# Performance work log

Hardware: AMD Instinct MI355X
Metric: run time of the kernel (lower is better)

Reference implementation:

```python
import jax, jax.numpy as jnp
import numpy as np

OUT_IMG = 256
OUT_MSK = 64


def _src_coords(n_out, size):
    # F.interpolate bilinear align_corners=False source coordinates, clamped to edge
    sizef = size.astype(jnp.float32)
    t = (jnp.arange(n_out, dtype=jnp.float32) + 0.5) * (sizef / n_out) - 0.5
    t = jnp.clip(t, 0.0, sizef - 1.0)
    t0 = jnp.floor(t).astype(jnp.int32)
    t1 = jnp.minimum(t0 + 1, size - 1)
    return t0, t1, t - t0.astype(jnp.float32)


def _per_sample(x_img, x_msk, x_bg, pad, sel, color):
    # x_img [3,H,W] float, x_msk [H,W] bool, x_bg [3,Hb,Wb], pad [4] int (l,r,t,b)
    H, W = x_msk.shape
    ys = jnp.any(x_msk, axis=1)
    xs = jnp.any(x_msk, axis=0)
    iy = jnp.arange(H)
    ix = jnp.arange(W)
    miny = jnp.min(jnp.where(ys, iy, H))
    maxy = jnp.max(jnp.where(ys, iy, -1))
    minx = jnp.min(jnp.where(xs, ix, W))
    maxx = jnp.max(jnp.where(xs, ix, -1))
    h = maxy - miny + 1
    w = maxx - minx + 1
    left, right, top, bot = pad[0], pad[1], pad[2], pad[3]
    Hp = h + top + bot   # padded crop height
    Wp = w + left + right  # padded crop width
    # background: real bg image or solid random color (c[ii][-1] > 2 branch)
    bg_sel = jnp.where(sel > 2, x_bg, jnp.broadcast_to(color[:, None, None], x_bg.shape))

    def mask_at(P, Q):
        # value of the padded-cropped mask at integer padded coords (P, Q)
        in_crop = (P >= top) & (P < top + h) & (Q >= left) & (Q < left + w)
        r = jnp.clip(miny + P - top, 0, H - 1)
        c = jnp.clip(minx + Q - left, 0, W - 1)
        return in_crop & x_msk[r, c], r, c

    def sample_img(py, px):
        # composited padded image at integer coords (py x px grid) -> [3,Ho,Wo]
        P = py[:, None]
        Q = px[None, :]
        m, r, c = mask_at(P, Q)
        iv = x_img[:, r, c]
        bv = bg_sel[:, P, Q]
        return jnp.where(m[None], iv, bv)

    def sample_msk(py, px):
        m, _, _ = mask_at(py[:, None], px[None, :])
        return m.astype(jnp.float32)

    def bilinear(sample_fn, n_out, ch_leading):
        y0, y1, wy = _src_coords(n_out, Hp)
        x0, x1, wx = _src_coords(n_out, Wp)
        s00 = sample_fn(y0, x0)
        s01 = sample_fn(y0, x1)
        s10 = sample_fn(y1, x0)
        s11 = sample_fn(y1, x1)
        wy_ = wy[:, None]
        wx_ = wx[None, :]
        if ch_leading:
            wy_ = wy_[None]
            wx_ = wx_[None]
        top_row = s00 * (1.0 - wx_) + s01 * wx_
        bot_row = s10 * (1.0 - wx_) + s11 * wx_
        return top_row * (1.0 - wy_) + bot_row * wy_

    img_out = bilinear(sample_img, OUT_IMG, True)        # [3,256,256]
    msk_out = bilinear(sample_msk, OUT_MSK, False)[None]  # [1,64,64]
    return img_out, msk_out


def _rgb_to_hsv(x):
    r, g, b = x[:, 0], x[:, 1], x[:, 2]
    mx = jnp.max(x, axis=1)
    mn = jnp.min(x, axis=1)
    d = mx - mn
    ds = jnp.where(d > 0, d, 1.0)
    hr = ((g - b) / ds) % 6.0
    hg = (b - r) / ds + 2.0
    hb = (r - g) / ds + 4.0
    hch = jnp.where(mx == r, hr, jnp.where(mx == g, hg, hb)) / 6.0
    hch = jnp.where(d > 0, hch, 0.0)
    s = jnp.where(mx > 0, d / jnp.where(mx > 0, mx, 1.0), 0.0)
    return hch, s, mx


def _hsv_to_rgb(hch, s, v):
    h6 = hch * 6.0
    i = jnp.floor(h6)
    f = h6 - i
    p = v * (1.0 - s)
    q = v * (1.0 - f * s)
    t = v * (1.0 - (1.0 - f) * s)
    im = i.astype(jnp.int32) % 6
    conds = [im == 0, im == 1, im == 2, im == 3, im == 4, im == 5]
    r = jnp.select(conds, [v, q, p, p, t, v])
    g = jnp.select(conds, [t, v, v, q, p, p])
    b = jnp.select(conds, [p, p, t, v, v, q])
    return jnp.stack([r, g, b], axis=1)


def _color_jitter(img, jit):
    # ColorJitter(0.1, 0.1, 0.1, 0.1) with explicit per-sample factors
    b = (0.9 + 0.2 * jit[:, 0])[:, None, None, None]
    c = (0.9 + 0.2 * jit[:, 1])[:, None, None, None]
    s = (0.9 + 0.2 * jit[:, 2])[:, None, None, None]
    hd = (-0.1 + 0.2 * jit[:, 3])[:, None, None]
    img = jnp.clip(img * b, 0.0, 1.0)
    gray = (0.299 * img[:, 0] + 0.587 * img[:, 1] + 0.114 * img[:, 2])[:, None]
    mean = jnp.mean(gray, axis=(2, 3), keepdims=True)
    img = jnp.clip(c * img + (1.0 - c) * mean, 0.0, 1.0)
    gray = (0.299 * img[:, 0] + 0.587 * img[:, 1] + 0.114 * img[:, 2])[:, None]
    img = jnp.clip(s * img + (1.0 - s) * gray, 0.0, 1.0)
    hch, sa, v = _rgb_to_hsv(img)
    hch = (hch + hd) % 1.0
    return jnp.clip(_hsv_to_rgb(hch, sa, v), 0.0, 1.0)


def setup_inputs() -> dict:
    key = jax.random.key(0)
    ks = jax.random.split(key, 7)
    B, H, W = 64, 448, 448
    return {
        "img": jax.random.uniform(ks[0], (B, 3, H, W), jnp.float32),
        "ms": jax.random.uniform(ks[1], (B, 1, H, W), jnp.float32),
        "bg": jax.random.uniform(ks[2], (B, 3, H + 40, W + 40), jnp.float32),
        "pads": jax.random.randint(ks[3], (B, 4), 0, 20, jnp.int32),
        "csel": jax.random.randint(ks[4], (B,), 0, 20, jnp.int32),
        "rand_color": jax.random.uniform(ks[5], (B, 3), jnp.float32),
        "jitter": jax.random.uniform(ks[6], (B, 4), jnp.float32),
    }


def reference(img, ms, bg, pads, csel, rand_color, jitter):
    mask = ms[:, 0] > 0.5
    img_out, msk_out = jax.vmap(_per_sample)(img, mask, bg, pads, csel, rand_color)
    img_out = _color_jitter(img_out, jitter)
    return img_out, msk_out
```

## Files before the change

kernel.cpp:

```cpp
#include <hip/hip_runtime.h>

#define H_IN 448
#define W_IN 448
#define HW_IN (H_IN * W_IN)
#define BGW 488
#define BGHW (BGW * BGW)
#define OUTI 256
#define OUTI_PIX (OUTI * OUTI)
#define OUTM 64
#define B_SAMPLES 64
#define BBOX_CHUNKS 16
#define BBOX_ROWS (H_IN / BBOX_CHUNKS)
#define BITS_STRIDE 8

typedef unsigned long long u64;

__device__ __forceinline__ float clamp01(float x) { return fminf(fmaxf(x, 0.f), 1.f); }
__device__ __forceinline__ int clampi(int x, int lo, int hi) { return min(max(x, lo), hi); }

__global__ void k_bbox(const float* __restrict__ ms, int* __restrict__ bbox,
                       u64* __restrict__ bits) {
    int b = blockIdx.y, chunk = blockIdx.x;
    int tid = threadIdx.x;
    int wave = tid >> 6, lane = tid & 63;
    const float* msB = ms + (size_t)b * HW_IN;
    u64* bitsB = bits + (size_t)b * H_IN * BITS_STRIDE;

    int miny = H_IN, maxy = -1, minx = W_IN, maxx = -1;
    for (int rr = wave; rr < BBOX_ROWS; rr += 4) {
        int row = chunk * BBOX_ROWS + rr;
        const float4* rowp = (const float4*)(msB + (size_t)row * W_IN);
#pragma unroll
        for (int sub = 0; sub < 2; ++sub) {
            int c4 = sub * 64 + lane;
            bool valid = c4 < (W_IN / 4);
            float4 v = rowp[min(c4, W_IN / 4 - 1)];
            bool a0 = valid && (v.x > 0.5f);
            bool a1 = valid && (v.y > 0.5f);
            bool a2 = valid && (v.z > 0.5f);
            bool a3 = valid && (v.w > 0.5f);
            u64 b0 = __ballot(a0), b1 = __ballot(a1), b2 = __ballot(a2), b3 = __ballot(a3);
            if (a0 | a1 | a2 | a3) {
                miny = min(miny, row); maxy = max(maxy, row);
                int xb = c4 * 4;
                if (a0) { minx = min(minx, xb);     maxx = max(maxx, xb); }
                if (a1) { minx = min(minx, xb + 1); maxx = max(maxx, xb + 1); }
                if (a2) { minx = min(minx, xb + 2); maxx = max(maxx, xb + 2); }
                if (a3) { minx = min(minx, xb + 3); maxx = max(maxx, xb + 3); }
            }
            if (lane < 4) {
                u64 w = (lane == 0) ? b0 : (lane == 1) ? b1 : (lane == 2) ? b2 : b3;
                bitsB[(size_t)row * BITS_STRIDE + sub * 4 + lane] = w;
            }
        }
    }
    __shared__ int s[4];
    if (tid == 0) { s[0] = H_IN; s[1] = -1; s[2] = W_IN; s[3] = -1; }
    __syncthreads();
    atomicMin(&s[0], miny); atomicMax(&s[1], maxy);
    atomicMin(&s[2], minx); atomicMax(&s[3], maxx);
    __syncthreads();
    if (tid == 0) {
        atomicMin(&bbox[b * 4 + 0], s[0]);
        atomicMin(&bbox[b * 4 + 1], -s[1]);
        atomicMin(&bbox[b * 4 + 2], s[2]);
        atomicMin(&bbox[b * 4 + 3], -s[3]);
    }
}

struct Geo {
    int miny, minx, h, w, top, left, Hp, Wp;
};
__device__ __forceinline__ Geo load_geo(const int* __restrict__ bbox,
                                        const int* __restrict__ pads, int b) {
    Geo g;
    g.miny = bbox[b * 4 + 0];
    int maxy = -bbox[b * 4 + 1];
    g.minx = bbox[b * 4 + 2];
    int maxx = -bbox[b * 4 + 3];
    int left = pads[b * 4 + 0], right = pads[b * 4 + 1];
    int top = pads[b * 4 + 2], bot = pads[b * 4 + 3];
    g.h = maxy - g.miny + 1;
    g.w = maxx - g.minx + 1;
    g.top = top; g.left = left;
    g.Hp = g.h + top + bot;
    g.Wp = g.w + left + right;
    return g;
}

__device__ __forceinline__ void src_coord(int i, int n_out, int size,
                                          int& t0, int& t1, float& frac) {
    float sizef = (float)size;
    float t = (i + 0.5f) * (sizef / (float)n_out) - 0.5f;
    t = fminf(fmaxf(t, 0.f), sizef - 1.f);
    t0 = (int)floorf(t);
    t1 = min(t0 + 1, size - 1);
    frac = t - (float)t0;
}

__device__ __forceinline__ bool mask_bit(const u64* rowbits, int c) {
    u64 w = rowbits[((c >> 8) << 2) | (c & 3)];
    return (w >> ((c >> 2) & 63)) & 1ULL;
}

__global__ void __launch_bounds__(256) k_resize_img(
        const float* __restrict__ img, const float* __restrict__ bg,
        const int* __restrict__ pads, const int* __restrict__ csel,
        const float* __restrict__ rcol, const float* __restrict__ jit,
        const int* __restrict__ bbox, const u64* __restrict__ bits,
        float* __restrict__ out, float* __restrict__ partials) {
    int oy = blockIdx.x;
    int ch = blockIdx.y;
    int b = blockIdx.z;
    int tid = threadIdx.x;

    Geo g = load_geo(bbox, pads, b);
    bool useBg = csel[b] > 2;
    float colv = rcol[b * 3 + ch];
    float bfac = 0.9f + 0.2f * jit[b * 4 + 0];

    int y0, y1; float wy;
    src_coord(oy, OUTI, g.Hp, y0, y1, wy);
    int r0 = clampi(g.miny + y0 - g.top, 0, H_IN - 1);
    int r1 = clampi(g.miny + y1 - g.top, 0, H_IN - 1);
    bool incy0 = (y0 >= g.top) && (y0 < g.top + g.h);
    bool incy1 = (y1 >= g.top) && (y1 < g.top + g.h);

    __shared__ float s_im[2][W_IN];
    __shared__ float s_bg[2][BGW];
    __shared__ u64 s_bits[2][BITS_STRIDE];

    const float* imC = img + ((size_t)b * 3 + ch) * HW_IN;
    const float* bgC = bg + ((size_t)b * 3 + ch) * BGHW;
    const u64* bitsB = bits + (size_t)b * H_IN * BITS_STRIDE;

    if (tid < 2 * (W_IN / 4)) {
        int ky = tid >= (W_IN / 4);
        int c4 = tid - ky * (W_IN / 4);
        ((float4*)s_im[ky])[c4] =
            ((const float4*)(imC + (size_t)(ky ? r1 : r0) * W_IN))[c4];
    }
    if (useBg && tid < 2 * (BGW / 4)) {
        int ky = tid >= (BGW / 4);
        int c4 = tid - ky * (BGW / 4);
        ((float4*)s_bg[ky])[c4] =
            ((const float4*)(bgC + (size_t)(ky ? y1 : y0) * BGW))[c4];
    }
    if (tid < 16) {
        int ky = tid >> 3, idx = tid & 7;
        s_bits[ky][idx] = bitsB[(size_t)(ky ? r1 : r0) * BITS_STRIDE + idx];
    }
    __syncthreads();

    int x0, x1; float wx;
    src_coord(tid, OUTI, g.Wp, x0, x1, wx);

    float acc = 0.f;
#pragma unroll
    for (int tap = 0; tap < 4; ++tap) {
        int ky = tap >> 1;
        int Q = (tap & 1) ? x1 : x0;
        float wgt = (ky ? wy : 1.f - wy) * ((tap & 1) ? wx : 1.f - wx);
        bool incy = ky ? incy1 : incy0;
        bool in_crop = incy && (Q >= g.left) && (Q < g.left + g.w);
        int c = clampi(g.minx + Q - g.left, 0, W_IN - 1);
        bool mm = in_crop && mask_bit(s_bits[ky], c);
        float v = mm ? s_im[ky][c] : (useBg ? s_bg[ky][Q] : colv);
        acc += wgt * v;
    }
    float o = clamp01(acc * bfac);
    out[((size_t)b * 3 + ch) * OUTI_PIX + (size_t)oy * OUTI + tid] = o;

    float gsum = o;
#pragma unroll
    for (int off = 32; off > 0; off >>= 1) gsum += __shfl_down(gsum, off, 64);
    __shared__ float ls[4];
    int wid = tid >> 6, lane = tid & 63;
    if (lane == 0) ls[wid] = gsum;
    __syncthreads();
    if (tid == 0)
        partials[((size_t)b * 3 + ch) * 256 + oy] = ls[0] + ls[1] + ls[2] + ls[3];
}

__global__ void k_resize_msk(const u64* __restrict__ bits, const int* __restrict__ pads,
                             const int* __restrict__ bbox, float* __restrict__ outm) {
    int b = blockIdx.y;
    int pix = blockIdx.x * blockDim.x + threadIdx.x;
    int oy = pix >> 6, ox = pix & 63;

    Geo g = load_geo(bbox, pads, b);
    int y0, y1, x0, x1; float wy, wx;
    src_coord(oy, OUTM, g.Hp, y0, y1, wy);
    src_coord(ox, OUTM, g.Wp, x0, x1, wx);

    const u64* bitsB = bits + (size_t)b * H_IN * BITS_STRIDE;
    float acc = 0.f;
#pragma unroll
    for (int tap = 0; tap < 4; ++tap) {
        int P = (tap & 2) ? y1 : y0;
        int Q = (tap & 1) ? x1 : x0;
        float wgt = ((tap & 2) ? wy : 1.f - wy) * ((tap & 1) ? wx : 1.f - wx);
        bool in_crop = (P >= g.top) && (P < g.top + g.h) && (Q >= g.left) && (Q < g.left + g.w);
        int r = clampi(g.miny + P - g.top, 0, H_IN - 1);
        int c = clampi(g.minx + Q - g.left, 0, W_IN - 1);
        bool mm = in_crop && mask_bit(bitsB + (size_t)r * BITS_STRIDE, c);
        acc += wgt * (mm ? 1.f : 0.f);
    }
    outm[(size_t)b * (OUTM * OUTM) + pix] = acc;
}

__device__ __forceinline__ void jitter_px(float& r, float& g, float& bl,
                                          float cc, float ssf, float hd, float mean) {
    r = clamp01(cc * r + (1.f - cc) * mean);
    g = clamp01(cc * g + (1.f - cc) * mean);
    bl = clamp01(cc * bl + (1.f - cc) * mean);
    float gray = 0.299f * r + 0.587f * g + 0.114f * bl;
    r = clamp01(ssf * r + (1.f - ssf) * gray);
    g = clamp01(ssf * g + (1.f - ssf) * gray);
    bl = clamp01(ssf * bl + (1.f - ssf) * gray);
    float mx = fmaxf(r, fmaxf(g, bl));
    float mn = fminf(r, fminf(g, bl));
    float d = mx - mn;
    float dsv = (d > 0.f) ? d : 1.f;
    float hch;
    if (mx == r) {
        float t = (g - bl) / dsv;
        t = fmodf(t, 6.f);
        if (t < 0.f) t += 6.f;
        hch = t;
    } else if (mx == g) {
        hch = (bl - r) / dsv + 2.f;
    } else {
        hch = (r - g) / dsv + 4.f;
    }
    hch = (d > 0.f) ? hch * (1.f / 6.f) : 0.f;
    float sat = (mx > 0.f) ? d / mx : 0.f;
    float v = mx;
    float hh = hch + hd;
    hh -= floorf(hh);
    float h6 = hh * 6.f;
    float fi = floorf(h6);
    float f = h6 - fi;
    float pp = v * (1.f - sat);
    float q = v * (1.f - f * sat);
    float t = v * (1.f - (1.f - f) * sat);
    int im = ((int)fi) % 6;
    float ro, go, bo;
    switch (im) {
        case 0: ro = v;  go = t;  bo = pp; break;
        case 1: ro = q;  go = v;  bo = pp; break;
        case 2: ro = pp; go = v;  bo = t;  break;
        case 3: ro = pp; go = q;  bo = v;  break;
        case 4: ro = t;  go = pp; bo = v;  break;
        default: ro = v; go = pp; bo = q;  break;
    }
    r = clamp01(ro); g = clamp01(go); bl = clamp01(bo);
}

__global__ void k_jitter(float* __restrict__ io, const float* __restrict__ jit,
                         const float* __restrict__ partials) {
    int b = blockIdx.y;
    int tid = threadIdx.x;

    float pv = 0.299f * partials[((size_t)b * 3 + 0) * 256 + tid]
             + 0.587f * partials[((size_t)b * 3 + 1) * 256 + tid]
             + 0.114f * partials[((size_t)b * 3 + 2) * 256 + tid];
#pragma unroll
    for (int off = 32; off > 0; off >>= 1) pv += __shfl_down(pv, off, 64);
    __shared__ float ls[4];
    int wid = tid >> 6, lane = tid & 63;
    if (lane == 0) ls[wid] = pv;
    __syncthreads();
    float mean = (ls[0] + ls[1] + ls[2] + ls[3]) * (1.f / (float)OUTI_PIX);

    float cc = 0.9f + 0.2f * jit[b * 4 + 1];
    float ssf = 0.9f + 0.2f * jit[b * 4 + 2];
    float hd = -0.1f + 0.2f * jit[b * 4 + 3];

    int idx4 = blockIdx.x * blockDim.x + tid;
    float4* pr = (float4*)(io + (size_t)b * 3 * OUTI_PIX) + idx4;
    float4* pg = pr + OUTI_PIX / 4;
    float4* pb = pr + 2 * (OUTI_PIX / 4);
    float4 r = *pr, g = *pg, bl = *pb;

    jitter_px(r.x, g.x, bl.x, cc, ssf, hd, mean);
    jitter_px(r.y, g.y, bl.y, cc, ssf, hd, mean);
    jitter_px(r.z, g.z, bl.z, cc, ssf, hd, mean);
    jitter_px(r.w, g.w, bl.w, cc, ssf, hd, mean);

    *pr = r; *pg = g; *pb = bl;
}

extern "C" void kernel_launch(void* const* d_in, const int* in_sizes, int n_in,
                              void* d_out, int out_size, void* d_ws, size_t ws_size,
                              hipStream_t stream) {
    const float* img = (const float*)d_in[0];
    const float* ms = (const float*)d_in[1];
    const float* bg = (const float*)d_in[2];
    const int* pads = (const int*)d_in[3];
    const int* csel = (const int*)d_in[4];
    const float* rcol = (const float*)d_in[5];
    const float* jit = (const float*)d_in[6];
    float* out = (float*)d_out;

    int* bbox = (int*)d_ws;
    float* partials = (float*)((char*)d_ws + 1024);
    u64* bits = (u64*)((char*)d_ws + 1024 + B_SAMPLES * 3 * 256 * sizeof(float));
    float* outm = out + (size_t)B_SAMPLES * 3 * OUTI_PIX;

    hipMemsetAsync(bbox, 0x7F, B_SAMPLES * 4 * sizeof(int), stream);

    k_bbox<<<dim3(BBOX_CHUNKS, B_SAMPLES), 256, 0, stream>>>(ms, bbox, bits);
    k_resize_img<<<dim3(OUTI, 3, B_SAMPLES), 256, 0, stream>>>(
        img, bg, pads, csel, rcol, jit, bbox, bits, out, partials);
    k_resize_msk<<<dim3((OUTM * OUTM) / 256, B_SAMPLES), 256, 0, stream>>>(
        bits, pads, bbox, outm);
    k_jitter<<<dim3(OUTI_PIX / 4 / 256, B_SAMPLES), 256, 0, stream>>>(out, jit, partials);
}
```

Baseline: 146.2 us.

## Process all three channels per block in image resize kernel

The resize kernel now handles all three color channels in one block instead of launching one block per channel. Geometry, mask bits and tap coordinates are computed once and shared across channels, and the luminance-weighted partial sum is formed in-kernel, so the jitter kernel reads one partial per row instead of three. In exchange each block uses about three times the shared memory and does more staging loads, which may lower occupancy, and the grid has a third as many blocks.

```diff
diff --git a/kernel.cpp b/kernel.cpp
--- a/kernel.cpp
+++ b/kernel.cpp
@@ -110,13 +110,12 @@
         const int* __restrict__ bbox, const u64* __restrict__ bits,
         float* __restrict__ out, float* __restrict__ partials) {
     int oy = blockIdx.x;
-    int ch = blockIdx.y;
-    int b = blockIdx.z;
+    int b = blockIdx.y;
     int tid = threadIdx.x;
 
     Geo g = load_geo(bbox, pads, b);
     bool useBg = csel[b] > 2;
-    float colv = rcol[b * 3 + ch];
+    float c0 = rcol[b * 3 + 0], c1 = rcol[b * 3 + 1], c2 = rcol[b * 3 + 2];
     float bfac = 0.9f + 0.2f * jit[b * 4 + 0];
 
     int y0, y1; float wy;
@@ -126,25 +125,41 @@
     bool incy0 = (y0 >= g.top) && (y0 < g.top + g.h);
     bool incy1 = (y1 >= g.top) && (y1 < g.top + g.h);
 
-    __shared__ float s_im[2][W_IN];
-    __shared__ float s_bg[2][BGW];
+    __shared__ float s_im[6][W_IN];
+    __shared__ float s_bg[6][BGW];
     __shared__ u64 s_bits[2][BITS_STRIDE];
 
-    const float* imC = img + ((size_t)b * 3 + ch) * HW_IN;
-    const float* bgC = bg + ((size_t)b * 3 + ch) * BGHW;
+    const float* imB = img + (size_t)b * 3 * HW_IN;
     const u64* bitsB = bits + (size_t)b * H_IN * BITS_STRIDE;
 
-    if (tid < 2 * (W_IN / 4)) {
-        int ky = tid >= (W_IN / 4);
-        int c4 = tid - ky * (W_IN / 4);
-        ((float4*)s_im[ky])[c4] =
-            ((const float4*)(imC + (size_t)(ky ? r1 : r0) * W_IN))[c4];
-    }
-    if (useBg && tid < 2 * (BGW / 4)) {
-        int ky = tid >= (BGW / 4);
-        int c4 = tid - ky * (BGW / 4);
-        ((float4*)s_bg[ky])[c4] =
-            ((const float4*)(bgC + (size_t)(ky ? y1 : y0) * BGW))[c4];
+#pragma unroll
+    for (int k = 0; k < 3; ++k) {
+        int item = k * 256 + tid;
+        int p = item >> 7;
+        int idx = item & 127;
+        if (idx < W_IN / 4) {
+            int ky = p > 2;
+            int ch = p - 3 * ky;
+            int row = ky ? r1 : r0;
+            ((float4*)s_im[p])[idx] =
+                ((const float4*)(imB + (size_t)ch * HW_IN + (size_t)row * W_IN))[idx];
+        }
+    }
+    if (useBg) {
+        const float* bgB = bg + (size_t)b * 3 * BGHW;
+#pragma unroll
+        for (int k = 0; k < 3; ++k) {
+            int item = k * 256 + tid;
+            int p = item >> 7;
+            int idx = item & 127;
+            if (idx < BGW / 4) {
+                int ky = p > 2;
+                int ch = p - 3 * ky;
+                int row = ky ? y1 : y0;
+                ((float4*)s_bg[p])[idx] =
+                    ((const float4*)(bgB + (size_t)ch * BGHW + (size_t)row * BGW))[idx];
+            }
+        }
     }
     if (tid < 16) {
         int ky = tid >> 3, idx = tid & 7;
@@ -155,23 +170,37 @@
     int x0, x1; float wx;
     src_coord(tid, OUTI, g.Wp, x0, x1, wx);
 
-    float acc = 0.f;
+    float acc0 = 0.f, acc1 = 0.f, acc2 = 0.f;
 #pragma unroll
     for (int tap = 0; tap < 4; ++tap) {
         int ky = tap >> 1;
+        int ky3 = ky * 3;
         int Q = (tap & 1) ? x1 : x0;
         float wgt = (ky ? wy : 1.f - wy) * ((tap & 1) ? wx : 1.f - wx);
         bool incy = ky ? incy1 : incy0;
         bool in_crop = incy && (Q >= g.left) && (Q < g.left + g.w);
         int c = clampi(g.minx + Q - g.left, 0, W_IN - 1);
         bool mm = in_crop && mask_bit(s_bits[ky], c);
-        float v = mm ? s_im[ky][c] : (useBg ? s_bg[ky][Q] : colv);
-        acc += wgt * v;
-    }
-    float o = clamp01(acc * bfac);
-    out[((size_t)b * 3 + ch) * OUTI_PIX + (size_t)oy * OUTI + tid] = o;
-
-    float gsum = o;
+        float i0 = s_im[ky3 + 0][c], i1 = s_im[ky3 + 1][c], i2 = s_im[ky3 + 2][c];
+        float b0, b1, b2;
+        if (useBg) {
+            b0 = s_bg[ky3 + 0][Q]; b1 = s_bg[ky3 + 1][Q]; b2 = s_bg[ky3 + 2][Q];
+        } else {
+            b0 = c0; b1 = c1; b2 = c2;
+        }
+        acc0 += wgt * (mm ? i0 : b0);
+        acc1 += wgt * (mm ? i1 : b1);
+        acc2 += wgt * (mm ? i2 : b2);
+    }
+    float o0 = clamp01(acc0 * bfac);
+    float o1 = clamp01(acc1 * bfac);
+    float o2 = clamp01(acc2 * bfac);
+    size_t o = (size_t)b * 3 * OUTI_PIX + (size_t)oy * OUTI + tid;
+    out[o] = o0;
+    out[o + OUTI_PIX] = o1;
+    out[o + 2 * OUTI_PIX] = o2;
+
+    float gsum = 0.299f * o0 + 0.587f * o1 + 0.114f * o2;
 #pragma unroll
     for (int off = 32; off > 0; off >>= 1) gsum += __shfl_down(gsum, off, 64);
     __shared__ float ls[4];
@@ -179,7 +208,7 @@
     if (lane == 0) ls[wid] = gsum;
     __syncthreads();
     if (tid == 0)
-        partials[((size_t)b * 3 + ch) * 256 + oy] = ls[0] + ls[1] + ls[2] + ls[3];
+        partials[b * 256 + oy] = ls[0] + ls[1] + ls[2] + ls[3];
 }
 
 __global__ void k_resize_msk(const u64* __restrict__ bits, const int* __restrict__ pads,
@@ -262,9 +291,7 @@
     int b = blockIdx.y;
     int tid = threadIdx.x;
 
-    float pv = 0.299f * partials[((size_t)b * 3 + 0) * 256 + tid]
-             + 0.587f * partials[((size_t)b * 3 + 1) * 256 + tid]
-             + 0.114f * partials[((size_t)b * 3 + 2) * 256 + tid];
+    float pv = partials[b * 256 + tid];
 #pragma unroll
     for (int off = 32; off > 0; off >>= 1) pv += __shfl_down(pv, off, 64);
     __shared__ float ls[4];
@@ -305,13 +332,13 @@
 
     int* bbox = (int*)d_ws;
     float* partials = (float*)((char*)d_ws + 1024);
-    u64* bits = (u64*)((char*)d_ws + 1024 + B_SAMPLES * 3 * 256 * sizeof(float));
+    u64* bits = (u64*)((char*)d_ws + 1024 + B_SAMPLES * 256 * sizeof(float));
     float* outm = out + (size_t)B_SAMPLES * 3 * OUTI_PIX;
 
     hipMemsetAsync(bbox, 0x7F, B_SAMPLES * 4 * sizeof(int), stream);
 
     k_bbox<<<dim3(BBOX_CHUNKS, B_SAMPLES), 256, 0, stream>>>(ms, bbox, bits);
-    k_resize_img<<<dim3(OUTI, 3, B_SAMPLES), 256, 0, stream>>>(
+    k_resize_img<<<dim3(OUTI, B_SAMPLES), 256, 0, stream>>>(
         img, bg, pads, csel, rcol, jit, bbox, bits, out, partials);
     k_resize_msk<<<dim3((OUTM * OUTM) / 256, B_SAMPLES), 256, 0, stream>>>(
         bits, pads, bbox, outm);
```

Result: faster. 123.1 us (-15.8%).
